# Kernel tuning notes

Measured on AMD Instinct MI355X. Metric: run time of the kernel, lower is better.

## Reference

```python
import jax, jax.numpy as jnp
import numpy as np

J = 116  # ROI count; c_in = 4*J = 464


def setup_inputs() -> dict:
    key = jax.random.key(0)
    ks = jax.random.split(key, 8)
    B = 131072
    F = jax.random.normal(ks[0], (B, 2, J), dtype=jnp.float32)
    S = jax.random.normal(ks[1], (B, 2, J), dtype=jnp.float32)
    def lin(k, fan_in, fan_out):
        bound = 1.0 / np.sqrt(fan_in)
        kw, kb = jax.random.split(k)
        W = jax.random.uniform(kw, (fan_in, fan_out), jnp.float32, -bound, bound)
        b = jax.random.uniform(kb, (fan_out,), jnp.float32, -bound, bound)
        return W, b
    W1, b1 = lin(ks[2], 4 * J, 64)
    W2, b2 = lin(ks[3], 64, 32)
    W3, b3 = lin(ks[4], 32, 2)
    return {"F": F, "S": S, "W1": W1, "b1": b1, "W2": W2, "b2": b2, "W3": W3, "b3": b3}


def reference(F, S, W1, b1, W2, b2, W3, b3):
    # einsum('bkj,bij->bjki') then mean over (k,i) factors into mean_k(F)*mean_i(S)
    # per (b,j): mean_{k,i} F[b,k,j]*S[b,i,j] = mean_k F[b,k,j] * mean_i S[b,i,j]
    g = jax.nn.sigmoid(jnp.mean(F, axis=1) * jnp.mean(S, axis=1))  # (b, j)
    g = g[:, None, :]                                              # broadcast over the 2 channels
    Fg = F * g
    Sg = S * g
    feat = jnp.concatenate((Fg, Sg), axis=1).reshape(F.shape[0], -1)  # (b, 4*J)
    h = jax.nn.relu(feat @ W1 + b1)
    h = jax.nn.relu(h @ W2 + b2)
    logits = h @ W3 + b3
    return jax.nn.softmax(logits, axis=1)
```

## Files before the change

kernel.cpp:

```cpp
#include <hip/hip_runtime.h>
#include <stdint.h>


typedef float    f4    __attribute__((ext_vector_type(4)));
typedef float    f32x4 __attribute__((ext_vector_type(4)));
typedef _Float16 h8    __attribute__((ext_vector_type(8)));

#define NSTEP 15

__global__ void prep_w1(const float* __restrict__ W1, _Float16* __restrict__ Wsp) {
  const int e  = blockIdx.x * 256 + threadIdx.x;
  const int t  = e >> 11;
  const int r  = e & 2047;
  const int n  = r & 63;
  const int kk = r >> 6;
  const int h  = kk >> 3;
  const int ee = kk & 7;
  const int s  = ee & 1;
  const int jp = ee >> 1;
  const int fam = h >> 1;
  const int j  = 8 * t + 4 * (h & 1) + jp;
  const int ko = 232 * fam + 116 * s + j;
  const float v = (j < 116) ? W1[ko * 64 + n] : 0.f;
  Wsp[t * 2048 + n * 32 + kk] = (_Float16)v;
}

__global__ __launch_bounds__(256, 4) void mricls_main(
    const float* __restrict__ F, const float* __restrict__ S,
    const float* __restrict__ b1, const float* __restrict__ W2,
    const float* __restrict__ b2, const float* __restrict__ W3,
    const float* __restrict__ b3, const _Float16* __restrict__ Wsp,
    float* __restrict__ out) {
  __shared__ __align__(16) float h1s[64][68];
  __shared__ __align__(16) float W2s[64][32];
  __shared__ __align__(16) float W3s[32][2];
  __shared__ __align__(16) float b1s[64];
  __shared__ __align__(16) float b2s[32];
  __shared__ float b3s[2];

  const int tid = threadIdx.x;
  const int l   = tid & 63;
  const int w   = tid >> 6;
  const int ml  = l & 15;
  const int h   = l >> 4;

  {
    const f4* W2v = (const f4*)W2;
    f4* W2sv = (f4*)W2s;
#pragma unroll
    for (int i = 0; i < 2; ++i) W2sv[tid + 256 * i] = W2v[tid + 256 * i];
    if (tid < 16) ((f4*)W3s)[tid] = ((const f4*)W3)[tid];
    if (tid < 16) ((f4*)b1s)[tid] = ((const f4*)b1)[tid];
    if (tid < 8)  ((f4*)b2s)[tid] = ((const f4*)b2)[tid];
    if (tid < 2)  b3s[tid] = b3[tid];
  }

  const long row = (long)blockIdx.x * 64 + w * 16 + ml;
  const float* arr = (h < 2) ? F : S;
  const float* bp  = arr + row * 232 + 4 * (h & 1);
  const float* bpt = arr + row * 232 + ((h & 1) ? 0 : 112);
  const char*  bptr = (const char*)Wsp + (ml * 64 + h * 16);

  f32x4 acc[4];
#pragma unroll
  for (int nt = 0; nt < 4; ++nt) acc[nt] = (f32x4){0.f, 0.f, 0.f, 0.f};

  f4 xb[4][2];
#pragma unroll
  for (int t = 0; t < 4; ++t) {
    xb[t][0] = *(const f4*)(bp + 8 * t);
    xb[t][1] = *(const f4*)(bp + 8 * t + 116);
  }
  h8 bq[2][4];
#pragma unroll
  for (int nt = 0; nt < 4; ++nt) bq[0][nt] = *(const h8*)(bptr + nt * 1024);
#pragma unroll
  for (int nt = 0; nt < 4; ++nt) bq[1][nt] = *(const h8*)(bptr + 4096 + nt * 1024);
  bptr += 8192;

#pragma unroll
  for (int t = 0; t < NSTEP; ++t) {
    f4 cx0 = xb[t & 3][0];
    f4 cx1 = xb[t & 3][1];
    if (t + 4 < 14) {
      xb[t & 3][0] = *(const f4*)(bp + 8 * (t + 4));
      xb[t & 3][1] = *(const f4*)(bp + 8 * (t + 4) + 116);
    } else if (t + 4 == 14) {
      xb[t & 3][0] = *(const f4*)(bpt);
      xb[t & 3][1] = *(const f4*)(bpt + 116);
    }
    if (t == 14) {
      const float zf = (h & 1) ? 0.f : 1.f;
#pragma unroll
      for (int e = 0; e < 4; ++e) { cx0[e] *= zf; cx1[e] *= zf; }
    }
    h8 a;
#pragma unroll
    for (int jp = 0; jp < 4; ++jp) {
      const float u = cx0[jp] + cx1[jp];
      const float v = __shfl_xor(u, 32);
      const float g = 1.f / (1.f + __expf(-0.25f * u * v));
      a[2 * jp]     = (_Float16)(cx0[jp] * g);
      a[2 * jp + 1] = (_Float16)(cx1[jp] * g);
    }
#pragma unroll
    for (int nt = 0; nt < 4; ++nt)
      acc[nt] = __builtin_amdgcn_mfma_f32_16x16x32_f16(a, bq[t & 1][nt], acc[nt], 0, 0, 0);
    if (t + 2 < NSTEP) {
#pragma unroll
      for (int nt = 0; nt < 4; ++nt) bq[t & 1][nt] = *(const h8*)(bptr + nt * 1024);
      bptr += 4096;
    }
  }

  __syncthreads();

#pragma unroll
  for (int nt = 0; nt < 4; ++nt) {
    const int n = nt * 16 + ml;
    const float bias = b1s[n];
#pragma unroll
    for (int r = 0; r < 4; ++r) {
      const int mm = w * 16 + h * 4 + r;
      h1s[mm][n] = fmaxf(acc[nt][r] + bias, 0.f);
    }
  }
  __syncthreads();

  const int m2 = tid >> 2;
  const int q  = tid & 3;
  float acc2[8];
#pragma unroll
  for (int e = 0; e < 8; ++e) acc2[e] = b2s[q * 8 + e];
#pragma unroll 8
  for (int k = 0; k < 64; ++k) {
    const float hk = h1s[m2][k];
    const f4 w0 = *(const f4*)&W2s[k][q * 8];
    const f4 w1 = *(const f4*)&W2s[k][q * 8 + 4];
    acc2[0] = fmaf(hk, w0[0], acc2[0]);
    acc2[1] = fmaf(hk, w0[1], acc2[1]);
    acc2[2] = fmaf(hk, w0[2], acc2[2]);
    acc2[3] = fmaf(hk, w0[3], acc2[3]);
    acc2[4] = fmaf(hk, w1[0], acc2[4]);
    acc2[5] = fmaf(hk, w1[1], acc2[5]);
    acc2[6] = fmaf(hk, w1[2], acc2[6]);
    acc2[7] = fmaf(hk, w1[3], acc2[7]);
  }
  float p0 = 0.f, p1 = 0.f;
#pragma unroll
  for (int e = 0; e < 8; ++e) {
    const float hv = fmaxf(acc2[e], 0.f);
    p0 = fmaf(hv, W3s[q * 8 + e][0], p0);
    p1 = fmaf(hv, W3s[q * 8 + e][1], p1);
  }
  p0 += __shfl_xor(p0, 1); p0 += __shfl_xor(p0, 2);
  p1 += __shfl_xor(p1, 1); p1 += __shfl_xor(p1, 2);
  if (q == 0) {
    const float l0 = p0 + b3s[0], l1 = p1 + b3s[1];
    const float mx = fmaxf(l0, l1);
    const float e0 = __expf(l0 - mx), e1 = __expf(l1 - mx);
    const float inv = 1.f / (e0 + e1);
    float2 o = make_float2(e0 * inv, e1 * inv);
    *(float2*)(out + ((long)blockIdx.x * 64 + m2) * 2) = o;
  }
}

extern "C" void kernel_launch(void* const* d_in, const int* in_sizes, int n_in,
                              void* d_out, int out_size, void* d_ws, size_t ws_size,
                              hipStream_t stream) {
  const float* F  = (const float*)d_in[0];
  const float* S  = (const float*)d_in[1];
  const float* W1 = (const float*)d_in[2];
  const float* b1 = (const float*)d_in[3];
  const float* W2 = (const float*)d_in[4];
  const float* b2 = (const float*)d_in[5];
  const float* W3 = (const float*)d_in[6];
  const float* b3 = (const float*)d_in[7];
  _Float16* Wsp = (_Float16*)d_ws;
  float* out = (float*)d_out;
  const int B = in_sizes[0] / 232;

  prep_w1<<<dim3(120), dim3(256), 0, stream>>>(W1, Wsp);
  mricls_main<<<dim3(B / 64), dim3(256), 0, stream>>>(F, S, b1, W2, b2, W3, b3,
                                                      (const _Float16*)Wsp, out);
}
```

Baseline: 326.0 us.

## Stage F/S tiles into LDS via async global_load_lds with 32-row blocks

Each block now bulk-copies its 32-row F and S tiles straight into LDS with global_load_lds, then computes the gate by reading both tensors from LDS instead of using register prefetch plus a cross-lane shuffle. Blocks shrink to 128 threads and 32 rows, and the h1 staging buffer is unioned with the input buffers. The goal is to replace many small strided global loads with wide, coalesced async transfers. In exchange, about 68KB of LDS per block limits occupancy to a few waves per CU, and loads no longer overlap compute inside a block. The last step also reads slightly past each row and relies on zero-padded weights.

```diff
diff --git a/kernel.cpp b/kernel.cpp
--- a/kernel.cpp
+++ b/kernel.cpp
@@ -25,13 +25,16 @@
   Wsp[t * 2048 + n * 32 + kk] = (_Float16)v;
 }
 
-__global__ __launch_bounds__(256, 4) void mricls_main(
+__global__ __launch_bounds__(128, 2) void mricls_main(
     const float* __restrict__ F, const float* __restrict__ S,
     const float* __restrict__ b1, const float* __restrict__ W2,
     const float* __restrict__ b2, const float* __restrict__ W3,
     const float* __restrict__ b3, const _Float16* __restrict__ Wsp,
     float* __restrict__ out) {
-  __shared__ __align__(16) float h1s[64][68];
+  __shared__ __align__(16) union {
+    struct { char f[29696]; char s[29696]; } buf;
+    float h1[32][68];
+  } U;
   __shared__ __align__(16) float W2s[64][32];
   __shared__ __align__(16) float W3s[32][2];
   __shared__ __align__(16) float b1s[64];
@@ -45,72 +48,65 @@
   const int h   = l >> 4;
 
   {
+    const char* gsrc = ((w == 0) ? (const char*)F : (const char*)S)
+                       + (size_t)blockIdx.x * 29696 + l * 16;
+    char* ldst = (w == 0) ? U.buf.f : U.buf.s;
+#pragma unroll
+    for (int g = 0; g < 29; ++g)
+      __builtin_amdgcn_global_load_lds(gsrc + g * 1024, ldst + g * 1024, 16, 0, 0);
+  }
+
+  {
     const f4* W2v = (const f4*)W2;
     f4* W2sv = (f4*)W2s;
 #pragma unroll
-    for (int i = 0; i < 2; ++i) W2sv[tid + 256 * i] = W2v[tid + 256 * i];
+    for (int i = 0; i < 4; ++i) W2sv[tid + 128 * i] = W2v[tid + 128 * i];
     if (tid < 16) ((f4*)W3s)[tid] = ((const f4*)W3)[tid];
     if (tid < 16) ((f4*)b1s)[tid] = ((const f4*)b1)[tid];
     if (tid < 8)  ((f4*)b2s)[tid] = ((const f4*)b2)[tid];
     if (tid < 2)  b3s[tid] = b3[tid];
   }
 
-  const long row = (long)blockIdx.x * 64 + w * 16 + ml;
-  const float* arr = (h < 2) ? F : S;
-  const float* bp  = arr + row * 232 + 4 * (h & 1);
-  const float* bpt = arr + row * 232 + ((h & 1) ? 0 : 112);
-  const char*  bptr = (const char*)Wsp + (ml * 64 + h * 16);
+  const char* bb = (const char*)Wsp + ml * 64 + h * 16;
+  h8 bq[2][4];
+#pragma unroll
+  for (int nt = 0; nt < 4; ++nt) bq[0][nt] = *(const h8*)(bb + nt * 1024);
+
+  asm volatile("s_waitcnt vmcnt(0)" ::: "memory");
+  __syncthreads();
+
+  const int r  = w * 16 + ml;
+  const int fam = h >> 1;
+  const char* xb = (fam ? U.buf.s : U.buf.f) + r * 928 + (h & 1) * 16;
+  const char* yb = (fam ? U.buf.f : U.buf.s) + r * 928 + (h & 1) * 16;
 
   f32x4 acc[4];
 #pragma unroll
   for (int nt = 0; nt < 4; ++nt) acc[nt] = (f32x4){0.f, 0.f, 0.f, 0.f};
 
-  f4 xb[4][2];
-#pragma unroll
-  for (int t = 0; t < 4; ++t) {
-    xb[t][0] = *(const f4*)(bp + 8 * t);
-    xb[t][1] = *(const f4*)(bp + 8 * t + 116);
-  }
-  h8 bq[2][4];
-#pragma unroll
-  for (int nt = 0; nt < 4; ++nt) bq[0][nt] = *(const h8*)(bptr + nt * 1024);
-#pragma unroll
-  for (int nt = 0; nt < 4; ++nt) bq[1][nt] = *(const h8*)(bptr + 4096 + nt * 1024);
-  bptr += 8192;
-
 #pragma unroll
   for (int t = 0; t < NSTEP; ++t) {
-    f4 cx0 = xb[t & 3][0];
-    f4 cx1 = xb[t & 3][1];
-    if (t + 4 < 14) {
-      xb[t & 3][0] = *(const f4*)(bp + 8 * (t + 4));
-      xb[t & 3][1] = *(const f4*)(bp + 8 * (t + 4) + 116);
-    } else if (t + 4 == 14) {
-      xb[t & 3][0] = *(const f4*)(bpt);
-      xb[t & 3][1] = *(const f4*)(bpt + 116);
+    if (t + 1 < NSTEP) {
+#pragma unroll
+      for (int nt = 0; nt < 4; ++nt)
+        bq[(t + 1) & 1][nt] = *(const h8*)(bb + (t + 1) * 4096 + nt * 1024);
     }
-    if (t == 14) {
-      const float zf = (h & 1) ? 0.f : 1.f;
-#pragma unroll
-      for (int e = 0; e < 4; ++e) { cx0[e] *= zf; cx1[e] *= zf; }
-    }
+    const f4 x0 = *(const f4*)(xb + t * 32);
+    const f4 x1 = *(const f4*)(xb + t * 32 + 464);
+    const f4 y0 = *(const f4*)(yb + t * 32);
+    const f4 y1 = *(const f4*)(yb + t * 32 + 464);
     h8 a;
 #pragma unroll
     for (int jp = 0; jp < 4; ++jp) {
-      const float u = cx0[jp] + cx1[jp];
-      const float v = __shfl_xor(u, 32);
+      const float u = x0[jp] + x1[jp];
+      const float v = y0[jp] + y1[jp];
       const float g = 1.f / (1.f + __expf(-0.25f * u * v));
-      a[2 * jp]     = (_Float16)(cx0[jp] * g);
-      a[2 * jp + 1] = (_Float16)(cx1[jp] * g);
+      a[2 * jp]     = (_Float16)(x0[jp] * g);
+      a[2 * jp + 1] = (_Float16)(x1[jp] * g);
     }
 #pragma unroll
     for (int nt = 0; nt < 4; ++nt)
       acc[nt] = __builtin_amdgcn_mfma_f32_16x16x32_f16(a, bq[t & 1][nt], acc[nt], 0, 0, 0);
-    if (t + 2 < NSTEP) {
-#pragma unroll
-      for (int nt = 0; nt < 4; ++nt) bq[t & 1][nt] = *(const h8*)(bptr + nt * 1024);
-      bptr += 4096;
-    }
   }
 
   __syncthreads();
@@ -120,12 +116,11 @@
     const int n = nt * 16 + ml;
     const float bias = b1s[n];
 #pragma unroll
-    for (int r = 0; r < 4; ++r) {
-      const int mm = w * 16 + h * 4 + r;
-      h1s[mm][n] = fmaxf(acc[nt][r] + bias, 0.f);
+    for (int rr = 0; rr < 4; ++rr) {
+      const int mm = w * 16 + h * 4 + rr;
+      U.h1[mm][n] = fmaxf(acc[nt][rr] + bias, 0.f);
     }
   }
-  __syncthreads();
 
   const int m2 = tid >> 2;
   const int q  = tid & 3;
@@ -134,7 +129,7 @@
   for (int e = 0; e < 8; ++e) acc2[e] = b2s[q * 8 + e];
 #pragma unroll 8
   for (int k = 0; k < 64; ++k) {
-    const float hk = h1s[m2][k];
+    const float hk = U.h1[m2][k];
     const f4 w0 = *(const f4*)&W2s[k][q * 8];
     const f4 w1 = *(const f4*)&W2s[k][q * 8 + 4];
     acc2[0] = fmaf(hk, w0[0], acc2[0]);
@@ -161,7 +156,7 @@
     const float e0 = __expf(l0 - mx), e1 = __expf(l1 - mx);
     const float inv = 1.f / (e0 + e1);
     float2 o = make_float2(e0 * inv, e1 * inv);
-    *(float2*)(out + ((long)blockIdx.x * 64 + m2) * 2) = o;
+    *(float2*)(out + ((long)blockIdx.x * 32 + m2) * 2) = o;
   }
 }
 
@@ -181,6 +176,6 @@
   const int B = in_sizes[0] / 232;
 
   prep_w1<<<dim3(120), dim3(256), 0, stream>>>(W1, Wsp);
-  mricls_main<<<dim3(B / 64), dim3(256), 0, stream>>>(F, S, b1, W2, b2, W3, b3,
+  mricls_main<<<dim3(B / 32), dim3(128), 0, stream>>>(F, S, b1, W2, b2, W3, b3,
                                                       (const _Float16*)Wsp, out);
 }
```

Measured after the change: 301.4 us. -7.6%, faster.
